# Kernel tuning notes

Measured on AMD Instinct MI355X. Metric: run time of the kernel, lower is better.

## Reference

```python
import jax, jax.numpy as jnp
import numpy as np

N_NODES = 50000
N_EDGES = 600000
D = 128
R = 8


def setup_inputs() -> dict:
    key = jax.random.key(0)
    ks = jax.random.split(key, 10)
    return {
        "node_ids": jnp.arange(N_NODES, dtype=jnp.int32),
        "src": jax.random.randint(ks[0], (N_EDGES,), 0, N_NODES, dtype=jnp.int32),
        "dst": jax.random.randint(ks[1], (N_EDGES,), 0, N_NODES, dtype=jnp.int32),
        "etype": jax.random.randint(ks[2], (N_EDGES,), 0, R, dtype=jnp.int32),
        "emb": jax.random.normal(ks[3], (N_NODES, D), dtype=jnp.float32) * 0.02,
        "W1": jax.random.normal(ks[4], (R, D, D), dtype=jnp.float32) * 0.05,
        "Wself1": jax.random.normal(ks[5], (D, D), dtype=jnp.float32) * 0.05,
        "b1": jnp.zeros((D,), dtype=jnp.float32),
        "W2": jax.random.normal(ks[6], (R, D, D), dtype=jnp.float32) * 0.05,
        "Wself2": jax.random.normal(ks[7], (D, D), dtype=jnp.float32) * 0.05,
        "b2": jnp.zeros((D,), dtype=jnp.float32),
    }


def rgcn_layer(h, W, Wself, b, src, dst, etype, n_nodes):
    # relation-wise transform of all node features: [R, N, d_out]
    hr = jnp.einsum('nd,rdo->rno', h, W)
    # per-edge gather of (relation, src) -> message, then scatter-sum to dst
    msgs = hr[etype, src]                                   # [E, d_out]
    agg = jax.ops.segment_sum(msgs, dst, num_segments=n_nodes)
    # self-loop + bias (activation=None, feat_drop=0)
    return agg + h @ Wself + b


def reference(node_ids, src, dst, etype, emb, W1, Wself1, b1, W2, Wself2, b2):
    h0 = emb[node_ids]                                      # embedding lookup over all nodes
    h1 = rgcn_layer(h0, W1, Wself1, b1, src, dst, etype, emb.shape[0])
    h2 = rgcn_layer(h1, W2, Wself2, b2, src, dst, etype, emb.shape[0])
    return h2
```

## Files before the change

### kernel.cpp

```cpp
#include <hip/hip_runtime.h>
#include <hip/hip_bf16.h>

#define NN 50000
#define NE 600000
#define DD 128
#define NR 8
#define NB (NN * NR)
#define NCHUNK8 ((NB + 255) / 256)
#define PERT ((NCHUNK8 + 255) / 256)

typedef __attribute__((ext_vector_type(8))) short bf16x8;
typedef __attribute__((ext_vector_type(4))) float f32x4;

__device__ __forceinline__ unsigned short f2bf(float f) {
  __hip_bfloat16 h = __float2bfloat16(f);
  return *reinterpret_cast<unsigned short*>(&h);
}
__device__ __forceinline__ unsigned pk2(float lo, float hi) {
  return (unsigned)f2bf(lo) | ((unsigned)f2bf(hi) << 16);
}
__device__ __forceinline__ float bflo(unsigned u) { return __uint_as_float(u << 16); }
__device__ __forceinline__ float bfhi(unsigned u) { return __uint_as_float(u & 0xffff0000u); }

__global__ __launch_bounds__(128) void convw_kernel(
    const float* __restrict__ W1, const float* __restrict__ Ws1,
    const float* __restrict__ W2, const float* __restrict__ Ws2,
    unsigned short* __restrict__ WT)
{
  const int m = blockIdx.y, o = blockIdx.x, d = threadIdx.x;
  const float* src;
  if (m < 8)       src = W1 + (size_t)m * DD * DD;
  else if (m == 8) src = Ws1;
  else if (m < 17) src = W2 + (size_t)(m - 9) * DD * DD;
  else             src = Ws2;
  WT[(size_t)m * DD * DD + o * DD + d] = f2bf(src[(size_t)d * DD + o]);
}

__global__ __launch_bounds__(256) void convh_kernel(
    const float* __restrict__ emb, const int* __restrict__ ids,
    unsigned short* __restrict__ h)
{
  const int gid = blockIdx.x * 256 + threadIdx.x;
  if (gid >= NN * 16) return;
  const int row = gid >> 4;
  const int off = (gid & 15) * 8;
  const int srcRow = ids[row];
  const float* src = emb + (size_t)srcRow * DD + off;
  const float4 a = *reinterpret_cast<const float4*>(src);
  const float4 b = *reinterpret_cast<const float4*>(src + 4);
  uint4 u;
  u.x = pk2(a.x, a.y); u.y = pk2(a.z, a.w);
  u.z = pk2(b.x, b.y); u.w = pk2(b.z, b.w);
  *reinterpret_cast<uint4*>(h + (size_t)row * DD + off) = u;
}

__global__ __launch_bounds__(256) void hist_kernel(
    const int* __restrict__ dst, const int* __restrict__ et,
    int* __restrict__ deg)
{
  const int e = blockIdx.x * 256 + threadIdx.x;
  if (e < NE) atomicAdd(&deg[dst[e] * NR + et[e]], 1);
}

__global__ __launch_bounds__(256) void bsum_kernel(
    const int* __restrict__ deg, int* __restrict__ bsum)
{
  __shared__ int tmp[256];
  const int t = threadIdx.x;
  const int i = blockIdx.x * 256 + t;
  tmp[t] = (i < NB) ? deg[i] : 0;
  __syncthreads();
#pragma unroll
  for (int off = 128; off > 0; off >>= 1) {
    if (t < off) tmp[t] += tmp[t + off];
    __syncthreads();
  }
  if (t == 0) bsum[blockIdx.x] = tmp[0];
}

__global__ __launch_bounds__(256) void bscan_kernel(
    const int* __restrict__ bsum, int* __restrict__ bbase)
{
  __shared__ int tmp[256];
  const int t = threadIdx.x;
  const int b = t * PERT;
  const int e = min(b + PERT, NCHUNK8);
  int s = 0;
  for (int i = b; i < e; ++i) s += bsum[i];
  tmp[t] = s;
  __syncthreads();
#pragma unroll
  for (int off = 1; off < 256; off <<= 1) {
    const int x = (t >= off) ? tmp[t - off] : 0;
    __syncthreads();
    tmp[t] += x;
    __syncthreads();
  }
  int run = tmp[t] - s;
  for (int i = b; i < e; ++i) {
    const int v = bsum[i];
    bbase[i] = run;
    run += v;
  }
}

__global__ __launch_bounds__(256) void expand_kernel(
    int* deg, const int* __restrict__ bbase, int* __restrict__ offsets)
{
  __shared__ int tmp[256];
  const int t = threadIdx.x;
  const int i = blockIdx.x * 256 + t;
  const int v = (i < NB) ? deg[i] : 0;
  tmp[t] = v;
  __syncthreads();
#pragma unroll
  for (int off = 1; off < 256; off <<= 1) {
    const int x = (t >= off) ? tmp[t - off] : 0;
    __syncthreads();
    tmp[t] += x;
    __syncthreads();
  }
  const int base = bbase[blockIdx.x];
  const int excl = base + tmp[t] - v;
  if (i < NB) {
    offsets[i] = excl;
    deg[i] = excl;
    if (i == NB - 1) offsets[NB] = base + tmp[t];
  }
}

__global__ __launch_bounds__(256) void fill_kernel(
    const int* __restrict__ src, const int* __restrict__ dst,
    const int* __restrict__ et, int* __restrict__ cursor,
    int* __restrict__ eidx)
{
  const int e = blockIdx.x * 256 + threadIdx.x;
  if (e < NE) {
    const int pos = atomicAdd(&cursor[dst[e] * NR + et[e]], 1);
    eidx[pos] = src[e];
  }
}

__device__ __forceinline__ void gather_frag(
    const unsigned short* __restrict__ h,
    const int* __restrict__ eidx,
    int beg, int end, int g, bf16x8* frag)
{
  float s[4][8];
#pragma unroll
  for (int ks = 0; ks < 4; ++ks)
#pragma unroll
    for (int j = 0; j < 8; ++j) s[ks][j] = 0.f;
  for (int i = beg; i < end; ++i) {
    const int srcn = eidx[i];
    const unsigned short* hp = h + (size_t)srcn * DD + g * 8;
#pragma unroll
    for (int ks = 0; ks < 4; ++ks) {
      const uint4 q = *reinterpret_cast<const uint4*>(hp + ks * 32);
      s[ks][0] += bflo(q.x); s[ks][1] += bfhi(q.x);
      s[ks][2] += bflo(q.y); s[ks][3] += bfhi(q.y);
      s[ks][4] += bflo(q.z); s[ks][5] += bfhi(q.z);
      s[ks][6] += bflo(q.w); s[ks][7] += bfhi(q.w);
    }
  }
#pragma unroll
  for (int ks = 0; ks < 4; ++ks) {
    uint4 u;
    u.x = pk2(s[ks][0], s[ks][1]);
    u.y = pk2(s[ks][2], s[ks][3]);
    u.z = pk2(s[ks][4], s[ks][5]);
    u.w = pk2(s[ks][6], s[ks][7]);
    frag[ks] = *reinterpret_cast<bf16x8*>(&u);
  }
}

template<int OUTF32>
__global__ __launch_bounds__(512, 4) void layer_kernel(
    const unsigned short* __restrict__ h,
    const int* __restrict__ off8, const int* __restrict__ eidx,
    const unsigned short* __restrict__ WTl,
    const float* __restrict__ bias,
    void* __restrict__ out)
{
  __shared__ __align__(16) char ldsW[2][DD * DD * 2];

  const int tid = threadIdx.x;
  const int rowBase = blockIdx.x * 128;
  const int lane = tid & 63;
  const int w = tid >> 6;
  const int c = lane & 15;
  const int g = lane >> 4;
  const int n = rowBase + w * 16 + c;
  const int nld = (n < NN) ? n : (NN - 1);

  int srcOff[4];
#pragma unroll
  for (int j = 0; j < 4; ++j) {
    const int dstB = (tid + j * 512) * 16;
    const int srcB = dstB ^ (((dstB >> 8) & 7) << 4);
    srcOff[j] = srcB >> 1;
  }

  uint4 wreg[4];
#pragma unroll
  for (int j = 0; j < 4; ++j)
    wreg[j] = *reinterpret_cast<const uint4*>(WTl + srcOff[j]);
#pragma unroll
  for (int j = 0; j < 4; ++j)
    *reinterpret_cast<uint4*>(ldsW[0] + (tid + j * 512) * 16) = wreg[j];

  bf16x8 fA[4], fB[4];
  gather_frag(h, eidx, off8[nld * NR], off8[nld * NR + 1], g, fA);

  f32x4 acc[8];
#pragma unroll
  for (int t = 0; t < 8; ++t) acc[t] = (f32x4){0.f, 0.f, 0.f, 0.f};

#define LSTEP(R, CUR, NXT)                                                            \
  {                                                                                   \
    __syncthreads();                                                                  \
    const char* buf = ldsW[(R) & 1];                                                  \
    if ((R) < NR) {                                                                   \
      const unsigned short* wnext = WTl + (size_t)((R) + 1) * DD * DD;                \
      _Pragma("unroll")                                                               \
      for (int j = 0; j < 4; ++j)                                                     \
        wreg[j] = *reinterpret_cast<const uint4*>(wnext + srcOff[j]);                 \
    }                                                                                 \
    _Pragma("unroll")                                                                 \
    for (int ks = 0; ks < 4; ++ks) {                                                  \
      _Pragma("unroll")                                                               \
      for (int t = 0; t < 8; ++t) {                                                   \
        const int addr = (((t * 16 + c) << 8) + (ks << 6) + (g << 4)) ^ ((c & 7) << 4); \
        bf16x8 a = *reinterpret_cast<const bf16x8*>(buf + addr);                      \
        acc[t] = __builtin_amdgcn_mfma_f32_16x16x32_bf16(a, CUR[ks], acc[t], 0, 0, 0); \
      }                                                                               \
    }                                                                                 \
    if ((R) < NR) {                                                                   \
      if ((R) + 1 < NR) {                                                             \
        gather_frag(h, eidx, off8[nld * NR + (R) + 1], off8[nld * NR + (R) + 2], g, NXT); \
      } else {                                                                        \
        _Pragma("unroll")                                                             \
        for (int ks = 0; ks < 4; ++ks)                                                \
          NXT[ks] = *reinterpret_cast<const bf16x8*>(h + (size_t)nld * DD + ks * 32 + g * 8); \
      }                                                                               \
      char* nbuf = ldsW[((R) & 1) ^ 1];                                               \
      _Pragma("unroll")                                                               \
      for (int j = 0; j < 4; ++j)                                                     \
        *reinterpret_cast<uint4*>(nbuf + (tid + j * 512) * 16) = wreg[j];             \
    }                                                                                 \
  }

  LSTEP(0, fA, fB) LSTEP(1, fB, fA) LSTEP(2, fA, fB) LSTEP(3, fB, fA)
  LSTEP(4, fA, fB) LSTEP(5, fB, fA) LSTEP(6, fA, fB) LSTEP(7, fB, fA)
  LSTEP(8, fA, fB)
#undef LSTEP

  if (n >= NN) return;
  if (OUTF32) {
    float* dst = (float*)out + (size_t)n * DD;
#pragma unroll
    for (int t = 0; t < 8; ++t) {
      const int o0 = t * 16 + g * 4;
      const float4 bv = *reinterpret_cast<const float4*>(bias + o0);
      float4 o;
      o.x = acc[t][0] + bv.x; o.y = acc[t][1] + bv.y;
      o.z = acc[t][2] + bv.z; o.w = acc[t][3] + bv.w;
      *reinterpret_cast<float4*>(dst + o0) = o;
    }
  } else {
    unsigned short* dst = (unsigned short*)out + (size_t)n * DD;
#pragma unroll
    for (int t = 0; t < 8; ++t) {
      const int o0 = t * 16 + g * 4;
      const float4 bv = *reinterpret_cast<const float4*>(bias + o0);
      uint2 q;
      q.x = pk2(acc[t][0] + bv.x, acc[t][1] + bv.y);
      q.y = pk2(acc[t][2] + bv.z, acc[t][3] + bv.w);
      *reinterpret_cast<uint2*>(dst + o0) = q;
    }
  }
}

extern "C" void kernel_launch(void* const* d_in, const int* in_sizes, int n_in,
                              void* d_out, int out_size, void* d_ws, size_t ws_size,
                              hipStream_t stream) {
  const int*   node_ids = (const int*)d_in[0];
  const int*   src   = (const int*)d_in[1];
  const int*   dst   = (const int*)d_in[2];
  const int*   etype = (const int*)d_in[3];
  const float* emb   = (const float*)d_in[4];
  const float* W1    = (const float*)d_in[5];
  const float* Ws1   = (const float*)d_in[6];
  const float* b1    = (const float*)d_in[7];
  const float* W2    = (const float*)d_in[8];
  const float* Ws2   = (const float*)d_in[9];
  const float* b2    = (const float*)d_in[10];

  char* p = (char*)d_ws;
  unsigned short* h0 = (unsigned short*)p;  p += (size_t)NN * DD * 2;
  unsigned short* h1 = (unsigned short*)p;  p += (size_t)NN * DD * 2;
  unsigned short* WT = (unsigned short*)p;  p += (size_t)18 * DD * DD * 2;
  int* off8          = (int*)p;             p += (size_t)(NB + 1) * 4;
  int* deg8          = (int*)p;             p += (size_t)NB * 4;
  int* eidx          = (int*)p;             p += (size_t)NE * 4;
  int* bsum          = (int*)p;             p += (size_t)NCHUNK8 * 4;
  int* bbase         = (int*)p;

  const int eb = (NE + 255) / 256;
  const int tb = (NN + 127) / 128;

  convw_kernel<<<dim3(DD, 18), 128, 0, stream>>>(W1, Ws1, W2, Ws2, WT);
  convh_kernel<<<(NN * 16) / 256, 256, 0, stream>>>(emb, node_ids, h0);
  hipMemsetAsync(deg8, 0, (size_t)NB * 4, stream);
  hist_kernel<<<eb, 256, 0, stream>>>(dst, etype, deg8);
  bsum_kernel<<<NCHUNK8, 256, 0, stream>>>(deg8, bsum);
  bscan_kernel<<<1, 256, 0, stream>>>(bsum, bbase);
  expand_kernel<<<NCHUNK8, 256, 0, stream>>>(deg8, bbase, off8);
  fill_kernel<<<eb, 256, 0, stream>>>(src, dst, etype, deg8, eidx);

  layer_kernel<0><<<tb, 512, 0, stream>>>(h0, off8, eidx, WT, b1, h1);
  layer_kernel<1><<<tb, 512, 0, stream>>>(h1, off8, eidx, WT + (size_t)9 * DD * DD, b2, (float*)d_out);
}
```

Before: 258.1 us.

## Single-buffer LDS weights, preload segment offsets and prefetch first edge indices

Halves the LDS weight buffer to a single 32KB slab with two barriers per relation step, which could let more blocks reside per CU. All nine CSR offsets per node are loaded up front, and the first four source indices of the next relation's edge list are fetched before the MFMA loop so their latency overlaps the compute. The per-relation gather is unrolled for up to four edges. In exchange, the weight load for the next relation is no longer overlapped with the MFMAs, and each step now needs an extra barrier.

```diff
diff --git a/kernel.cpp b/kernel.cpp
--- a/kernel.cpp
+++ b/kernel.cpp
@@ -141,28 +141,34 @@
   }
 }
 
-__device__ __forceinline__ void gather_frag(
-    const unsigned short* __restrict__ h,
-    const int* __restrict__ eidx,
-    int beg, int end, int g, bf16x8* frag)
+__device__ __forceinline__ void gacc_row(
+    const unsigned short* __restrict__ h, int idx, int g, float s[4][8])
+{
+  const unsigned short* hp = h + (size_t)idx * DD + g * 8;
+#pragma unroll
+  for (int ks = 0; ks < 4; ++ks) {
+    const uint4 q = *reinterpret_cast<const uint4*>(hp + ks * 32);
+    s[ks][0] += bflo(q.x); s[ks][1] += bfhi(q.x);
+    s[ks][2] += bflo(q.y); s[ks][3] += bfhi(q.y);
+    s[ks][4] += bflo(q.z); s[ks][5] += bfhi(q.z);
+    s[ks][6] += bflo(q.w); s[ks][7] += bfhi(q.w);
+  }
+}
+
+__device__ __forceinline__ void gather_accum(
+    const unsigned short* __restrict__ h, const int* __restrict__ eidx,
+    int pb, int ne, int pe0, int pe1, int pe2, int pe3, int g, bf16x8* frag)
 {
   float s[4][8];
 #pragma unroll
   for (int ks = 0; ks < 4; ++ks)
 #pragma unroll
     for (int j = 0; j < 8; ++j) s[ks][j] = 0.f;
-  for (int i = beg; i < end; ++i) {
-    const int srcn = eidx[i];
-    const unsigned short* hp = h + (size_t)srcn * DD + g * 8;
-#pragma unroll
-    for (int ks = 0; ks < 4; ++ks) {
-      const uint4 q = *reinterpret_cast<const uint4*>(hp + ks * 32);
-      s[ks][0] += bflo(q.x); s[ks][1] += bfhi(q.x);
-      s[ks][2] += bflo(q.y); s[ks][3] += bfhi(q.y);
-      s[ks][4] += bflo(q.z); s[ks][5] += bfhi(q.z);
-      s[ks][6] += bflo(q.w); s[ks][7] += bfhi(q.w);
-    }
-  }
+  if (ne > 0) gacc_row(h, pe0, g, s);
+  if (ne > 1) gacc_row(h, pe1, g, s);
+  if (ne > 2) gacc_row(h, pe2, g, s);
+  if (ne > 3) gacc_row(h, pe3, g, s);
+  for (int j = 4; j < ne; ++j) gacc_row(h, eidx[pb + j], g, s);
 #pragma unroll
   for (int ks = 0; ks < 4; ++ks) {
     uint4 u;
@@ -182,7 +188,7 @@
     const float* __restrict__ bias,
     void* __restrict__ out)
 {
-  __shared__ __align__(16) char ldsW[2][DD * DD * 2];
+  __shared__ __align__(16) char ldsW[DD * DD * 2];
 
   const int tid = threadIdx.x;
   const int rowBase = blockIdx.x * 128;
@@ -201,16 +207,29 @@
     srcOff[j] = srcB >> 1;
   }
 
+  int ob[9];
+#pragma unroll
+  for (int k = 0; k < 9; ++k) ob[k] = off8[nld * NR + k];
+
   uint4 wreg[4];
 #pragma unroll
   for (int j = 0; j < 4; ++j)
     wreg[j] = *reinterpret_cast<const uint4*>(WTl + srcOff[j]);
+
+  bf16x8 fA[4], fB[4];
+  {
+    const int pb = ob[0], ne = ob[1] - ob[0];
+    const int pe0 = eidx[min(pb + 0, NE - 1)];
+    const int pe1 = eidx[min(pb + 1, NE - 1)];
+    const int pe2 = eidx[min(pb + 2, NE - 1)];
+    const int pe3 = eidx[min(pb + 3, NE - 1)];
+    gather_accum(h, eidx, pb, ne, pe0, pe1, pe2, pe3, g, fA);
+  }
+
 #pragma unroll
   for (int j = 0; j < 4; ++j)
-    *reinterpret_cast<uint4*>(ldsW[0] + (tid + j * 512) * 16) = wreg[j];
-
-  bf16x8 fA[4], fB[4];
-  gather_frag(h, eidx, off8[nld * NR], off8[nld * NR + 1], g, fA);
+    *reinterpret_cast<uint4*>(ldsW + (tid + j * 512) * 16) = wreg[j];
+  __syncthreads();
 
   f32x4 acc[8];
 #pragma unroll
@@ -218,35 +237,40 @@
 
 #define LSTEP(R, CUR, NXT)                                                            \
   {                                                                                   \
-    __syncthreads();                                                                  \
-    const char* buf = ldsW[(R) & 1];                                                  \
-    if ((R) < NR) {                                                                   \
-      const unsigned short* wnext = WTl + (size_t)((R) + 1) * DD * DD;                \
-      _Pragma("unroll")                                                               \
-      for (int j = 0; j < 4; ++j)                                                     \
-        wreg[j] = *reinterpret_cast<const uint4*>(wnext + srcOff[j]);                 \
+    int pb = 0, pne = 0, pe0 = 0, pe1 = 0, pe2 = 0, pe3 = 0;                          \
+    if ((R) + 1 < NR) {                                                               \
+      pb = ob[(R) + 1]; pne = ob[(R) + 2] - pb;                                       \
+      pe0 = eidx[min(pb + 0, NE - 1)];                                                \
+      pe1 = eidx[min(pb + 1, NE - 1)];                                                \
+      pe2 = eidx[min(pb + 2, NE - 1)];                                                \
+      pe3 = eidx[min(pb + 3, NE - 1)];                                                \
     }                                                                                 \
     _Pragma("unroll")                                                                 \
     for (int ks = 0; ks < 4; ++ks) {                                                  \
       _Pragma("unroll")                                                               \
       for (int t = 0; t < 8; ++t) {                                                   \
         const int addr = (((t * 16 + c) << 8) + (ks << 6) + (g << 4)) ^ ((c & 7) << 4); \
-        bf16x8 a = *reinterpret_cast<const bf16x8*>(buf + addr);                      \
+        bf16x8 a = *reinterpret_cast<const bf16x8*>(ldsW + addr);                     \
         acc[t] = __builtin_amdgcn_mfma_f32_16x16x32_bf16(a, CUR[ks], acc[t], 0, 0, 0); \
       }                                                                               \
     }                                                                                 \
+    if ((R) + 1 < NR) {                                                               \
+      gather_accum(h, eidx, pb, pne, pe0, pe1, pe2, pe3, g, NXT);                     \
+    } else if ((R) == NR - 1) {                                                       \
+      _Pragma("unroll")                                                               \
+      for (int ks = 0; ks < 4; ++ks)                                                  \
+        NXT[ks] = *reinterpret_cast<const bf16x8*>(h + (size_t)nld * DD + ks * 32 + g * 8); \
+    }                                                                                 \
     if ((R) < NR) {                                                                   \
-      if ((R) + 1 < NR) {                                                             \
-        gather_frag(h, eidx, off8[nld * NR + (R) + 1], off8[nld * NR + (R) + 2], g, NXT); \
-      } else {                                                                        \
-        _Pragma("unroll")                                                             \
-        for (int ks = 0; ks < 4; ++ks)                                                \
-          NXT[ks] = *reinterpret_cast<const bf16x8*>(h + (size_t)nld * DD + ks * 32 + g * 8); \
-      }                                                                               \
-      char* nbuf = ldsW[((R) & 1) ^ 1];                                               \
+      const unsigned short* wnext = WTl + (size_t)((R) + 1) * DD * DD;                \
       _Pragma("unroll")                                                               \
       for (int j = 0; j < 4; ++j)                                                     \
-        *reinterpret_cast<uint4*>(nbuf + (tid + j * 512) * 16) = wreg[j];             \
+        wreg[j] = *reinterpret_cast<const uint4*>(wnext + srcOff[j]);                 \
+      __syncthreads();                                                                \
+      _Pragma("unroll")                                                               \
+      for (int j = 0; j < 4; ++j)                                                     \
+        *reinterpret_cast<uint4*>(ldsW + (tid + j * 512) * 16) = wreg[j];             \
+      __syncthreads();                                                                \
     }                                                                                 \
   }
 
```

Measured after the change: 318.2 us. 23.3% more time.

## Halve layer block to 64 rows and stream weights in half-K LDS phases

Applied to the files above, without the earlier changes.

The layer kernel now runs 256-thread blocks covering 64 destination rows, and stages each 128x128 weight matrix through LDS in two 64-column halves. This gives 18 pipeline phases instead of 9. LDS use per block drops from 64KB to 32KB, which should let more blocks stay resident and hide the latency of the irregular neighbor gathers. The segment offsets for the next gather are loaded early, and the gather loop is moved into a helper. The cost is twice as many barriers and weight reloads per row, and every block re-reads the full weight set for half as many rows.

```diff
diff --git a/kernel.cpp b/kernel.cpp
--- a/kernel.cpp
+++ b/kernel.cpp
@@ -141,6 +141,20 @@
   }
 }
 
+__device__ __forceinline__ void gacc_row(
+    const unsigned short* __restrict__ h, int idx, int g, float s[4][8])
+{
+  const unsigned short* hp = h + (size_t)idx * DD + g * 8;
+#pragma unroll
+  for (int ks = 0; ks < 4; ++ks) {
+    const uint4 q = *reinterpret_cast<const uint4*>(hp + ks * 32);
+    s[ks][0] += bflo(q.x); s[ks][1] += bfhi(q.x);
+    s[ks][2] += bflo(q.y); s[ks][3] += bfhi(q.y);
+    s[ks][4] += bflo(q.z); s[ks][5] += bfhi(q.z);
+    s[ks][6] += bflo(q.w); s[ks][7] += bfhi(q.w);
+  }
+}
+
 __device__ __forceinline__ void gather_frag(
     const unsigned short* __restrict__ h,
     const int* __restrict__ eidx,
@@ -151,18 +165,7 @@
   for (int ks = 0; ks < 4; ++ks)
 #pragma unroll
     for (int j = 0; j < 8; ++j) s[ks][j] = 0.f;
-  for (int i = beg; i < end; ++i) {
-    const int srcn = eidx[i];
-    const unsigned short* hp = h + (size_t)srcn * DD + g * 8;
-#pragma unroll
-    for (int ks = 0; ks < 4; ++ks) {
-      const uint4 q = *reinterpret_cast<const uint4*>(hp + ks * 32);
-      s[ks][0] += bflo(q.x); s[ks][1] += bfhi(q.x);
-      s[ks][2] += bflo(q.y); s[ks][3] += bfhi(q.y);
-      s[ks][4] += bflo(q.z); s[ks][5] += bfhi(q.z);
-      s[ks][6] += bflo(q.w); s[ks][7] += bfhi(q.w);
-    }
-  }
+  for (int i = beg; i < end; ++i) gacc_row(h, eidx[i], g, s);
 #pragma unroll
   for (int ks = 0; ks < 4; ++ks) {
     uint4 u;
@@ -175,17 +178,17 @@
 }
 
 template<int OUTF32>
-__global__ __launch_bounds__(512, 4) void layer_kernel(
+__global__ __launch_bounds__(256, 4) void layer_kernel(
     const unsigned short* __restrict__ h,
     const int* __restrict__ off8, const int* __restrict__ eidx,
     const unsigned short* __restrict__ WTl,
     const float* __restrict__ bias,
     void* __restrict__ out)
 {
-  __shared__ __align__(16) char ldsW[2][DD * DD * 2];
+  __shared__ __align__(16) char ldsW[2][DD * 64 * 2];
 
   const int tid = threadIdx.x;
-  const int rowBase = blockIdx.x * 128;
+  const int rowBase = blockIdx.x * 64;
   const int lane = tid & 63;
   const int w = tid >> 6;
   const int c = lane & 15;
@@ -193,67 +196,82 @@
   const int n = rowBase + w * 16 + c;
   const int nld = (n < NN) ? n : (NN - 1);
 
-  int srcOff[4];
+  int dstB[4], srcRel[4];
 #pragma unroll
   for (int j = 0; j < 4; ++j) {
-    const int dstB = (tid + j * 512) * 16;
-    const int srcB = dstB ^ (((dstB >> 8) & 7) << 4);
-    srcOff[j] = srcB >> 1;
-  }
-
-  uint4 wreg[4];
-#pragma unroll
-  for (int j = 0; j < 4; ++j)
-    wreg[j] = *reinterpret_cast<const uint4*>(WTl + srcOff[j]);
-#pragma unroll
-  for (int j = 0; j < 4; ++j)
-    *reinterpret_cast<uint4*>(ldsW[0] + (tid + j * 512) * 16) = wreg[j];
+    const int i = tid + j * 256;
+    const int o = i >> 3, slot = i & 7;
+    dstB[j] = ((o << 7) | (slot << 4)) ^ ((o & 7) << 4);
+    srcRel[j] = o * DD + slot * 8;
+  }
 
   bf16x8 fA[4], fB[4];
   gather_frag(h, eidx, off8[nld * NR], off8[nld * NR + 1], g, fA);
 
+  uint4 wreg[4];
+#pragma unroll
+  for (int j = 0; j < 4; ++j)
+    wreg[j] = *reinterpret_cast<const uint4*>(WTl + srcRel[j]);
+#pragma unroll
+  for (int j = 0; j < 4; ++j)
+    *reinterpret_cast<uint4*>(ldsW[0] + dstB[j]) = wreg[j];
+
   f32x4 acc[8];
 #pragma unroll
   for (int t = 0; t < 8; ++t) acc[t] = (f32x4){0.f, 0.f, 0.f, 0.f};
 
-#define LSTEP(R, CUR, NXT)                                                            \
+#define PH(P, CUR, NXT)                                                               \
   {                                                                                   \
     __syncthreads();                                                                  \
-    const char* buf = ldsW[(R) & 1];                                                  \
-    if ((R) < NR) {                                                                   \
-      const unsigned short* wnext = WTl + (size_t)((R) + 1) * DD * DD;                \
+    if ((P) < 17) {                                                                   \
+      const unsigned short* wsrc = WTl                                                \
+          + (size_t)(((P) + 1) >> 1) * DD * DD + (((P) + 1) & 1) * 64;                \
       _Pragma("unroll")                                                               \
       for (int j = 0; j < 4; ++j)                                                     \
-        wreg[j] = *reinterpret_cast<const uint4*>(wnext + srcOff[j]);                 \
+        wreg[j] = *reinterpret_cast<const uint4*>(wsrc + srcRel[j]);                  \
+    }                                                                                 \
+    int gb = 0, ge = 0;                                                               \
+    if (((P) & 1) == 0 && ((P) >> 1) + 1 < NR) {                                      \
+      gb = off8[nld * NR + ((P) >> 1) + 1];                                           \
+      ge = off8[nld * NR + ((P) >> 1) + 2];                                           \
     }                                                                                 \
     _Pragma("unroll")                                                                 \
-    for (int ks = 0; ks < 4; ++ks) {                                                  \
+    for (int kl = 0; kl < 2; ++kl) {                                                  \
       _Pragma("unroll")                                                               \
       for (int t = 0; t < 8; ++t) {                                                   \
-        const int addr = (((t * 16 + c) << 8) + (ks << 6) + (g << 4)) ^ ((c & 7) << 4); \
-        bf16x8 a = *reinterpret_cast<const bf16x8*>(buf + addr);                      \
-        acc[t] = __builtin_amdgcn_mfma_f32_16x16x32_bf16(a, CUR[ks], acc[t], 0, 0, 0); \
+        const int addr = (((t * 16 + c) << 7) + ((kl * 4 + g) << 4)) ^ ((c & 7) << 4); \
+        bf16x8 a = *reinterpret_cast<const bf16x8*>(ldsW[(P) & 1] + addr);            \
+        acc[t] = __builtin_amdgcn_mfma_f32_16x16x32_bf16(                             \
+            a, CUR[((P) & 1) * 2 + kl], acc[t], 0, 0, 0);                             \
       }                                                                               \
     }                                                                                 \
-    if ((R) < NR) {                                                                   \
-      if ((R) + 1 < NR) {                                                             \
-        gather_frag(h, eidx, off8[nld * NR + (R) + 1], off8[nld * NR + (R) + 2], g, NXT); \
-      } else {                                                                        \
+    if (((P) & 1) == 0) {                                                             \
+      if (((P) >> 1) + 1 < NR) {                                                      \
+        gather_frag(h, eidx, gb, ge, g, NXT);                                         \
+      } else if (((P) >> 1) + 1 == NR) {                                              \
         _Pragma("unroll")                                                             \
         for (int ks = 0; ks < 4; ++ks)                                                \
-          NXT[ks] = *reinterpret_cast<const bf16x8*>(h + (size_t)nld * DD + ks * 32 + g * 8); \
+          NXT[ks] = *reinterpret_cast<const bf16x8*>(                                 \
+              h + (size_t)nld * DD + ks * 32 + g * 8);                                \
       }                                                                               \
-      char* nbuf = ldsW[((R) & 1) ^ 1];                                               \
+    }                                                                                 \
+    if ((P) < 17) {                                                                   \
       _Pragma("unroll")                                                               \
       for (int j = 0; j < 4; ++j)                                                     \
-        *reinterpret_cast<uint4*>(nbuf + (tid + j * 512) * 16) = wreg[j];             \
-    }                                                                                 \
-  }
-
-  LSTEP(0, fA, fB) LSTEP(1, fB, fA) LSTEP(2, fA, fB) LSTEP(3, fB, fA)
-  LSTEP(4, fA, fB) LSTEP(5, fB, fA) LSTEP(6, fA, fB) LSTEP(7, fB, fA)
-  LSTEP(8, fA, fB)
-#undef LSTEP
+        *reinterpret_cast<uint4*>(ldsW[((P) + 1) & 1] + dstB[j]) = wreg[j];           \
+    }                                                                                 \
+  }
+
+  PH(0, fA, fB)  PH(1, fA, fB)
+  PH(2, fB, fA)  PH(3, fB, fA)
+  PH(4, fA, fB)  PH(5, fA, fB)
+  PH(6, fB, fA)  PH(7, fB, fA)
+  PH(8, fA, fB)  PH(9, fA, fB)
+  PH(10, fB, fA) PH(11, fB, fA)
+  PH(12, fA, fB) PH(13, fA, fB)
+  PH(14, fB, fA) PH(15, fB, fA)
+  PH(16, fA, fB) PH(17, fA, fB)
+#undef PH
 
   if (n >= NN) return;
   if (OUTF32) {
@@ -307,7 +325,7 @@
   int* bbase         = (int*)p;
 
   const int eb = (NE + 255) / 256;
-  const int tb = (NN + 127) / 128;
+  const int tb = (NN + 63) / 64;
 
   convw_kernel<<<dim3(DD, 18), 128, 0, stream>>>(W1, Ws1, W2, Ws2, WT);
   convh_kernel<<<(NN * 16) / 256, 256, 0, stream>>>(emb, node_ids, h0);
@@ -318,6 +336,6 @@
   expand_kernel<<<NCHUNK8, 256, 0, stream>>>(deg8, bbase, off8);
   fill_kernel<<<eb, 256, 0, stream>>>(src, dst, etype, deg8, eidx);
 
-  layer_kernel<0><<<tb, 512, 0, stream>>>(h0, off8, eidx, WT, b1, h1);
-  layer_kernel<1><<<tb, 512, 0, stream>>>(h1, off8, eidx, WT + (size_t)9 * DD * DD, b2, (float*)d_out);
-}
+  layer_kernel<0><<<tb, 256, 0, stream>>>(h0, off8, eidx, WT, b1, h1);
+  layer_kernel<1><<<tb, 256, 0, stream>>>(h1, off8, eidx, WT + (size_t)9 * DD * DD, b2, (float*)d_out);
+}
```

After: 252.0 us. 1.02x faster.
